# Kernel optimization log

Hardware: AMD Instinct MI355X
Metric: run time of the kernel (lower is better)

## Reference

```python
import jax, jax.numpy as jnp
import numpy as np

N_WAY = 64
N_SUPPORT = 1024   # 64-way, 16-shot
N_QUERY = 2048
IN_DIM = 49152     # 3*128*128 flattened RGB image
EMB = 2048
EPS = 1e-6         # torch CosineSimilarity eps


def setup_inputs() -> dict:
    key = jax.random.key(0)
    k1, k2, k3, k4 = jax.random.split(key, 4)
    support_images = jax.random.normal(k1, (N_SUPPORT, IN_DIM), dtype=jnp.float32)
    query_images = jax.random.normal(k2, (N_QUERY, IN_DIM), dtype=jnp.float32)
    # every class present => n_way = len(unique(labels)) = 64, as in the torch module
    support_labels = jnp.arange(N_SUPPORT, dtype=jnp.int64 if jax.config.jax_enable_x64 else jnp.int32) % N_WAY
    # linear backbone params (fan-in scaled)
    W = jax.random.normal(k3, (IN_DIM, EMB), dtype=jnp.float32) / np.sqrt(IN_DIM)
    b = jax.random.normal(k4, (EMB,), dtype=jnp.float32) * 0.01
    return {"support_images": support_images, "support_labels": support_labels,
            "query_images": query_images, "W": W, "b": b}


def reference(support_images, support_labels, query_images, W, b):
    # backbone encode (one big GEMM each)
    z_support = support_images @ W + b          # [Ns, E]
    z_query = query_images @ W + b              # [Nq, E]
    # per-class mean prototypes (replaces the python list-comprehension over labels)
    sums = jax.ops.segment_sum(z_support, support_labels, num_segments=N_WAY)      # [n_way, E]
    counts = jax.ops.segment_sum(jnp.ones((z_support.shape[0],), z_support.dtype),
                                 support_labels, num_segments=N_WAY)               # [n_way]
    z_proto = sums / counts[:, None]
    # pairwise cosine similarity (replaces the rs*cs python double loop)
    # torch: dot(a,b) / max(||a||*||b||, eps)
    q_norm = jnp.linalg.norm(z_query, axis=1)   # [Nq]
    p_norm = jnp.linalg.norm(z_proto, axis=1)   # [n_way]
    dots = z_query @ z_proto.T                  # [Nq, n_way]
    cscores = dots / jnp.maximum(q_norm[:, None] * p_norm[None, :], EPS)
    return cscores
```

## Files before the change

kernel.cpp:

```cpp
#include <hip/hip_runtime.h>
#include <hip/hip_bf16.h>
#include <stdint.h>

#define K_IN 49152
#define EMB  2048
#define NQ   2048
#define NS   1024
#define NW   64
#define MA   2176
#define MV   2112

typedef __bf16 bf16x8 __attribute__((ext_vector_type(8)));
typedef float  f32x4  __attribute__((ext_vector_type(4)));

__device__ __forceinline__ unsigned short f2bf(float f) {
  union { float f; uint32_t u; } v; v.f = f;
  uint32_t u = v.u;
  return (unsigned short)((u + 0x7FFFu + ((u >> 16) & 1u)) >> 16);
}

#define GLDS16(g, l) __builtin_amdgcn_global_load_lds( \
    (__attribute__((address_space(1))) void*)(g),      \
    (__attribute__((address_space(3))) void*)(l), 16, 0, 0)

__global__ void k_build_index(const int* __restrict__ labels, int* __restrict__ rowsIdx,
                              int* __restrict__ counts) {
  int t = threadIdx.x;
  if (t < NW) counts[t] = 0;
  __syncthreads();
  if (t < NS) {
    int lab = labels[t];
    int pos = atomicAdd(&counts[lab], 1);
    if (pos < 16) rowsIdx[lab * 16 + pos] = t;
  }
}

__global__ void k_proto_mean(const float* __restrict__ sup, const int* __restrict__ rowsIdx,
                             const int* __restrict__ counts, unsigned short* __restrict__ Abf) {
  int c = blockIdx.y;
  int d0 = blockIdx.x * 1024 + threadIdx.x * 4;
  float4 s = make_float4(0.f, 0.f, 0.f, 0.f);
  int cnt = counts[c]; if (cnt > 16) cnt = 16;
  for (int j = 0; j < cnt; ++j) {
    int r = rowsIdx[c * 16 + j];
    float4 v = *(const float4*)(sup + (size_t)r * K_IN + d0);
    s.x += v.x; s.y += v.y; s.z += v.z; s.w += v.w;
  }
  float inv = 1.0f / (float)cnt;
  ushort4 o;
  o.x = f2bf(s.x * inv); o.y = f2bf(s.y * inv);
  o.z = f2bf(s.z * inv); o.w = f2bf(s.w * inv);
  *(ushort4*)(Abf + (size_t)(NQ + c) * K_IN + d0) = o;
}

__global__ void k_convert_q(const float* __restrict__ q, unsigned short* __restrict__ Abf) {
  size_t i4 = (size_t)blockIdx.x * blockDim.x + threadIdx.x;
  float4 v = *((const float4*)q + i4);
  ushort4 o; o.x = f2bf(v.x); o.y = f2bf(v.y); o.z = f2bf(v.z); o.w = f2bf(v.w);
  *((ushort4*)Abf + i4) = o;
}

__global__ void k_transpose_w(const float* __restrict__ W, unsigned short* __restrict__ Wt) {
  __shared__ float tile[64][65];
  int t = threadIdx.x;
  int k0 = blockIdx.x * 64, n0 = blockIdx.y * 64;
  int nl = t & 63, kb = (t >> 6) * 16;
  for (int r = 0; r < 16; ++r)
    tile[kb + r][nl] = W[(size_t)(k0 + kb + r) * EMB + n0 + nl];
  __syncthreads();
  int k2 = (t & 31) * 2, nb = (t >> 5) * 8;
  for (int r = 0; r < 8; ++r) {
    int n = nb + r;
    uint32_t lo = f2bf(tile[k2][n]);
    uint32_t hi = f2bf(tile[k2 + 1][n]);
    *(uint32_t*)(Wt + (size_t)(n0 + n) * K_IN + k0 + k2) = lo | (hi << 16);
  }
}

__global__ void k_zero(float* __restrict__ Z, int n4) {
  int i = blockIdx.x * blockDim.x + threadIdx.x;
  if (i < n4) ((float4*)Z)[i] = make_float4(0.f, 0.f, 0.f, 0.f);
}

__global__ __launch_bounds__(256, 3) void k_gemm(
    const unsigned short* __restrict__ Abf, const unsigned short* __restrict__ Wt,
    const float* __restrict__ bias, float* __restrict__ Z) {
  __shared__ unsigned short As[128 * 32];
  __shared__ unsigned short Bs[128 * 32];
  int tid = threadIdx.x;
  int rowBase = blockIdx.y * 128;
  int colBase = blockIdx.x * 128;
  int kbase   = blockIdx.z * (K_IN / 3);

  int r0 = tid >> 2;
  int kg = (tid & 3) * 8;
  const unsigned short* gA0 = Abf + (size_t)(rowBase + r0) * K_IN + kbase + kg;
  const unsigned short* gA1 = gA0 + (size_t)64 * K_IN;
  const unsigned short* gB0 = Wt  + (size_t)(colBase + r0) * K_IN + kbase + kg;
  const unsigned short* gB1 = gB0 + (size_t)64 * K_IN;
  unsigned short* lA0 = &As[r0 * 32 + kg];
  unsigned short* lA1 = &As[(64 + r0) * 32 + kg];
  unsigned short* lB0 = &Bs[r0 * 32 + kg];
  unsigned short* lB1 = &Bs[(64 + r0) * 32 + kg];

  int lane = tid & 63, wid = tid >> 6;
  int wm = wid >> 1, wn = wid & 1;
  int lrow = lane & 15, kgrp = (lane >> 4) * 8;
  const unsigned short* fa = &As[(wm * 64 + lrow) * 32 + kgrp];
  const unsigned short* fb = &Bs[(wn * 64 + lrow) * 32 + kgrp];

  f32x4 acc[4][4] = {};

  for (int kt = 0; kt < (K_IN / 3) / 32; ++kt) {
    int ko = kt * 32;
    GLDS16(gA0 + ko, lA0);
    GLDS16(gA1 + ko, lA1);
    GLDS16(gB0 + ko, lB0);
    GLDS16(gB1 + ko, lB1);
    __syncthreads();
    bf16x8 a[4], bb[4];
#pragma unroll
    for (int i = 0; i < 4; ++i) {
      a[i]  = *(const bf16x8*)(fa + i * 16 * 32);
      bb[i] = *(const bf16x8*)(fb + i * 16 * 32);
    }
#pragma unroll
    for (int i = 0; i < 4; ++i)
#pragma unroll
      for (int j = 0; j < 4; ++j)
        acc[i][j] = __builtin_amdgcn_mfma_f32_16x16x32_bf16(a[i], bb[j], acc[i][j], 0, 0, 0);
    __syncthreads();
  }

  int lquad = lane >> 4;
  bool addB = (blockIdx.z == 0);
#pragma unroll
  for (int i = 0; i < 4; ++i) {
#pragma unroll
    for (int j = 0; j < 4; ++j) {
      int m0 = rowBase + wm * 64 + i * 16 + lquad * 4;
      int n  = colBase + wn * 64 + j * 16 + lrow;
      float bv = addB ? bias[n] : 0.0f;
#pragma unroll
      for (int r = 0; r < 4; ++r)
        atomicAdd(&Z[(size_t)(m0 + r) * EMB + n], acc[i][j][r] + bv);
    }
  }
}

__global__ void k_norms(const float* __restrict__ Z, float* __restrict__ norms) {
  int wid = threadIdx.x >> 6, lane = threadIdx.x & 63;
  int row = blockIdx.x * 4 + wid;
  const float4* Zr = (const float4*)(Z + (size_t)row * EMB);
  float s = 0.f;
  for (int i = lane; i < EMB / 4; i += 64) {
    float4 v = Zr[i];
    s += v.x * v.x + v.y * v.y + v.z * v.z + v.w * v.w;
  }
  for (int d = 32; d > 0; d >>= 1) s += __shfl_down(s, d, 64);
  if (lane == 0) norms[row] = sqrtf(s);
}

__global__ void k_cosine(const float* __restrict__ Z, const float* __restrict__ norms,
                         float* __restrict__ out) {
  __shared__ float4 zq[4 * 512];
  int t = threadIdx.x;
  int q0 = blockIdx.x * 4;
  const float4* Z4 = (const float4*)Z;
  for (int v = 0; v < 8; ++v) {
    int idx = v * 256 + t;
    zq[idx] = Z4[(size_t)q0 * 512 + idx];
  }
  __syncthreads();
  int c = t & 63, qi = t >> 6;
  const float4* Zp = Z4 + (size_t)(NQ + c) * 512;
  const float4* Zq = &zq[qi * 512];
  float s = 0.f;
  for (int kv = 0; kv < 512; ++kv) {
    float4 p = Zp[kv];
    float4 q = Zq[kv];
    s += p.x * q.x + p.y * q.y + p.z * q.z + p.w * q.w;
  }
  float nq = norms[q0 + qi], np = norms[NQ + c];
  out[(size_t)(q0 + qi) * NW + c] = s / fmaxf(nq * np, 1e-6f);
}

extern "C" void kernel_launch(void* const* d_in, const int* in_sizes, int n_in,
                              void* d_out, int out_size, void* d_ws, size_t ws_size,
                              hipStream_t stream) {
  const float* sup    = (const float*)d_in[0];
  const int*   labels = (const int*)d_in[1];
  const float* qry    = (const float*)d_in[2];
  const float* W      = (const float*)d_in[3];
  const float* bias   = (const float*)d_in[4];
  float* out = (float*)d_out;

  char* w = (char*)d_ws;
  unsigned short* Abf = (unsigned short*)w;
  unsigned short* Wt  = (unsigned short*)(w + 213909504u);
  float* Z     = (float*)(w + 415236096u);
  float* norms = (float*)(w + 433061888u);
  int* rowsIdx = (int*)(w + 433070336u);
  int* counts  = (int*)(w + 433074432u);

  k_build_index<<<1, 1024, 0, stream>>>(labels, rowsIdx, counts);
  k_proto_mean<<<dim3(48, 64), 256, 0, stream>>>(sup, rowsIdx, counts, Abf);
  k_convert_q<<<98304, 256, 0, stream>>>(qry, Abf);
  k_transpose_w<<<dim3(768, 32), 256, 0, stream>>>(W, Wt);
  k_zero<<<(MA * EMB / 4 + 255) / 256, 256, 0, stream>>>(Z, MA * EMB / 4);
  k_gemm<<<dim3(16, 17, 3), 256, 0, stream>>>(Abf, Wt, bias, Z);
  k_norms<<<528, 256, 0, stream>>>(Z, norms);
  k_cosine<<<512, 256, 0, stream>>>(Z, norms, out);
}
```

Before: 1.868 ms.

## Widen GEMM K-tile with swizzled LDS, raise split-K, fuse norms into cosine

```diff
diff --git a/kernel.cpp b/kernel.cpp
--- a/kernel.cpp
+++ b/kernel.cpp
@@ -9,6 +9,7 @@
 #define NW   64
 #define MA   2176
 #define MV   2112
+#define EPS  1e-6f
 
 typedef __bf16 bf16x8 __attribute__((ext_vector_type(8)));
 typedef float  f32x4  __attribute__((ext_vector_type(4)));
@@ -82,53 +83,60 @@
   if (i < n4) ((float4*)Z)[i] = make_float4(0.f, 0.f, 0.f, 0.f);
 }
 
-__global__ __launch_bounds__(256, 3) void k_gemm(
+__global__ __launch_bounds__(256, 4) void k_gemm(
     const unsigned short* __restrict__ Abf, const unsigned short* __restrict__ Wt,
     const float* __restrict__ bias, float* __restrict__ Z) {
-  __shared__ unsigned short As[128 * 32];
-  __shared__ unsigned short Bs[128 * 32];
+  __shared__ unsigned short As[128 * 64];
+  __shared__ unsigned short Bs[128 * 64];
   int tid = threadIdx.x;
   int rowBase = blockIdx.y * 128;
   int colBase = blockIdx.x * 128;
-  int kbase   = blockIdx.z * (K_IN / 3);
-
-  int r0 = tid >> 2;
-  int kg = (tid & 3) * 8;
-  const unsigned short* gA0 = Abf + (size_t)(rowBase + r0) * K_IN + kbase + kg;
-  const unsigned short* gA1 = gA0 + (size_t)64 * K_IN;
-  const unsigned short* gB0 = Wt  + (size_t)(colBase + r0) * K_IN + kbase + kg;
-  const unsigned short* gB1 = gB0 + (size_t)64 * K_IN;
-  unsigned short* lA0 = &As[r0 * 32 + kg];
-  unsigned short* lA1 = &As[(64 + r0) * 32 + kg];
-  unsigned short* lB0 = &Bs[r0 * 32 + kg];
-  unsigned short* lB1 = &Bs[(64 + r0) * 32 + kg];
+  int kbase   = blockIdx.z * (K_IN / 6);
+
+  int rs   = tid >> 3;
+  int slot = tid & 7;
+  int gg   = slot ^ (rs & 7);
+  const unsigned short* gA = Abf + (size_t)(rowBase + rs) * K_IN + kbase + gg * 8;
+  const unsigned short* gB = Wt  + (size_t)(colBase + rs) * K_IN + kbase + gg * 8;
+  unsigned short* lA = &As[tid * 8];
+  unsigned short* lB = &Bs[tid * 8];
+  const size_t rstep = (size_t)32 * K_IN;
 
   int lane = tid & 63, wid = tid >> 6;
   int wm = wid >> 1, wn = wid & 1;
-  int lrow = lane & 15, kgrp = (lane >> 4) * 8;
-  const unsigned short* fa = &As[(wm * 64 + lrow) * 32 + kgrp];
-  const unsigned short* fb = &Bs[(wn * 64 + lrow) * 32 + kgrp];
+  int lrow = lane & 15, q = lane >> 4;
+  int key = lrow & 7;
 
   f32x4 acc[4][4] = {};
 
-  for (int kt = 0; kt < (K_IN / 3) / 32; ++kt) {
-    int ko = kt * 32;
-    GLDS16(gA0 + ko, lA0);
-    GLDS16(gA1 + ko, lA1);
-    GLDS16(gB0 + ko, lB0);
-    GLDS16(gB1 + ko, lB1);
-    __syncthreads();
-    bf16x8 a[4], bb[4];
-#pragma unroll
-    for (int i = 0; i < 4; ++i) {
-      a[i]  = *(const bf16x8*)(fa + i * 16 * 32);
-      bb[i] = *(const bf16x8*)(fb + i * 16 * 32);
-    }
-#pragma unroll
-    for (int i = 0; i < 4; ++i)
-#pragma unroll
-      for (int j = 0; j < 4; ++j)
-        acc[i][j] = __builtin_amdgcn_mfma_f32_16x16x32_bf16(a[i], bb[j], acc[i][j], 0, 0, 0);
+  for (int kt = 0; kt < 128; ++kt) {
+    int ko = kt * 64;
+    GLDS16(gA + ko,             lA);
+    GLDS16(gA + ko + rstep,     lA + 2048);
+    GLDS16(gA + ko + 2 * rstep, lA + 4096);
+    GLDS16(gA + ko + 3 * rstep, lA + 6144);
+    GLDS16(gB + ko,             lB);
+    GLDS16(gB + ko + rstep,     lB + 2048);
+    GLDS16(gB + ko + 2 * rstep, lB + 4096);
+    GLDS16(gB + ko + 3 * rstep, lB + 6144);
+    __syncthreads();
+#pragma unroll
+    for (int kk = 0; kk < 2; ++kk) {
+      bf16x8 a[4], bb[4];
+      int sl = (kk * 4 + q) ^ key;
+#pragma unroll
+      for (int i = 0; i < 4; ++i) {
+        int rowA = wm * 64 + i * 16 + lrow;
+        int rowB = wn * 64 + i * 16 + lrow;
+        a[i]  = *(const bf16x8*)(&As[rowA * 64 + sl * 8]);
+        bb[i] = *(const bf16x8*)(&Bs[rowB * 64 + sl * 8]);
+      }
+#pragma unroll
+      for (int i = 0; i < 4; ++i)
+#pragma unroll
+        for (int j = 0; j < 4; ++j)
+          acc[i][j] = __builtin_amdgcn_mfma_f32_16x16x32_bf16(a[i], bb[j], acc[i][j], 0, 0, 0);
+    }
     __syncthreads();
   }
 
@@ -148,41 +156,47 @@
   }
 }
 
-__global__ void k_norms(const float* __restrict__ Z, float* __restrict__ norms) {
-  int wid = threadIdx.x >> 6, lane = threadIdx.x & 63;
-  int row = blockIdx.x * 4 + wid;
-  const float4* Zr = (const float4*)(Z + (size_t)row * EMB);
-  float s = 0.f;
-  for (int i = lane; i < EMB / 4; i += 64) {
-    float4 v = Zr[i];
-    s += v.x * v.x + v.y * v.y + v.z * v.z + v.w * v.w;
-  }
-  for (int d = 32; d > 0; d >>= 1) s += __shfl_down(s, d, 64);
-  if (lane == 0) norms[row] = sqrtf(s);
-}
-
-__global__ void k_cosine(const float* __restrict__ Z, const float* __restrict__ norms,
-                         float* __restrict__ out) {
-  __shared__ float4 zq[4 * 512];
+__global__ __launch_bounds__(256) void k_cosine(const float* __restrict__ Z,
+                                                float* __restrict__ out) {
+  __shared__ float Ps[64][132];
+  __shared__ float Qs[8][132];
   int t = threadIdx.x;
-  int q0 = blockIdx.x * 4;
-  const float4* Z4 = (const float4*)Z;
-  for (int v = 0; v < 8; ++v) {
-    int idx = v * 256 + t;
-    zq[idx] = Z4[(size_t)q0 * 512 + idx];
-  }
-  __syncthreads();
-  int c = t & 63, qi = t >> 6;
-  const float4* Zp = Z4 + (size_t)(NQ + c) * 512;
-  const float4* Zq = &zq[qi * 512];
-  float s = 0.f;
-  for (int kv = 0; kv < 512; ++kv) {
-    float4 p = Zp[kv];
-    float4 q = Zq[kv];
-    s += p.x * q.x + p.y * q.y + p.z * q.z + p.w * q.w;
-  }
-  float nq = norms[q0 + qi], np = norms[NQ + c];
-  out[(size_t)(q0 + qi) * NW + c] = s / fmaxf(nq * np, 1e-6f);
+  int q0 = blockIdx.x * 8;
+  int qi = t >> 5;
+  int c  = t & 31;
+
+  float dot0 = 0.f, dot1 = 0.f, qn = 0.f, pn0 = 0.f, pn1 = 0.f;
+
+  for (int kc = 0; kc < EMB; kc += 128) {
+    __syncthreads();
+#pragma unroll
+    for (int j = 0; j < 8; ++j) {
+      int f = j * 256 + t;
+      int row = f >> 5, col4 = f & 31;
+      float4 v = *(const float4*)(Z + (size_t)(NQ + row) * EMB + kc + col4 * 4);
+      *(float4*)&Ps[row][col4 * 4] = v;
+    }
+    {
+      int row = t >> 5, col4 = t & 31;
+      float4 v = *(const float4*)(Z + (size_t)(q0 + row) * EMB + kc + col4 * 4);
+      *(float4*)&Qs[row][col4 * 4] = v;
+    }
+    __syncthreads();
+#pragma unroll 4
+    for (int kk = 0; kk < 32; ++kk) {
+      float4 qv = *(const float4*)&Qs[qi][kk * 4];
+      float4 p0 = *(const float4*)&Ps[c][kk * 4];
+      float4 p1 = *(const float4*)&Ps[c + 32][kk * 4];
+      dot0 += qv.x * p0.x + qv.y * p0.y + qv.z * p0.z + qv.w * p0.w;
+      dot1 += qv.x * p1.x + qv.y * p1.y + qv.z * p1.z + qv.w * p1.w;
+      qn   += qv.x * qv.x + qv.y * qv.y + qv.z * qv.z + qv.w * qv.w;
+      pn0  += p0.x * p0.x + p0.y * p0.y + p0.z * p0.z + p0.w * p0.w;
+      pn1  += p1.x * p1.x + p1.y * p1.y + p1.z * p1.z + p1.w * p1.w;
+    }
+  }
+  float nq = sqrtf(qn);
+  out[(size_t)(q0 + qi) * NW + c]      = dot0 / fmaxf(nq * sqrtf(pn0), EPS);
+  out[(size_t)(q0 + qi) * NW + c + 32] = dot1 / fmaxf(nq * sqrtf(pn1), EPS);
 }
 
 extern "C" void kernel_launch(void* const* d_in, const int* in_sizes, int n_in,
@@ -199,7 +213,6 @@
   unsigned short* Abf = (unsigned short*)w;
   unsigned short* Wt  = (unsigned short*)(w + 213909504u);
   float* Z     = (float*)(w + 415236096u);
-  float* norms = (float*)(w + 433061888u);
   int* rowsIdx = (int*)(w + 433070336u);
   int* counts  = (int*)(w + 433074432u);
 
@@ -208,7 +221,6 @@
   k_convert_q<<<98304, 256, 0, stream>>>(qry, Abf);
   k_transpose_w<<<dim3(768, 32), 256, 0, stream>>>(W, Wt);
   k_zero<<<(MA * EMB / 4 + 255) / 256, 256, 0, stream>>>(Z, MA * EMB / 4);
-  k_gemm<<<dim3(16, 17, 3), 256, 0, stream>>>(Abf, Wt, bias, Z);
-  k_norms<<<528, 256, 0, stream>>>(Z, norms);
-  k_cosine<<<512, 256, 0, stream>>>(Z, norms, out);
-}
+  k_gemm<<<dim3(16, 17, 6), 256, 0, stream>>>(Abf, Wt, bias, Z);
+  k_cosine<<<256, 256, 0, stream>>>(Z, out);
+}
```

New measurement: 1.526 ms. 1.22x faster.
